# Kernel tuning notes

Hardware: AMD Instinct MI355X
Metric: run time of the kernel (lower is better)

## Reference

```python
import jax, jax.numpy as jnp
import numpy as np

B, T, C, NH = 8, 1024, 768, 12
HD = C // NH
NEG = -1e9


def setup_inputs() -> dict:
    key = jax.random.key(0)
    ks = jax.random.split(key, 8)
    s_c = 1.0 / np.sqrt(C)
    s_t = 1.0 / np.sqrt(T)
    return {
        "x": jax.random.normal(ks[0], (B, T, C), dtype=jnp.float32),
        "Wv": jax.random.normal(ks[1], (C, C), dtype=jnp.float32) * s_c,
        "bv": jnp.zeros((C,), dtype=jnp.float32),
        "Wl": jax.random.normal(ks[2], (T, T), dtype=jnp.float32) * s_t,  # weights_layer, no bias
        "Wc": jax.random.normal(ks[3], (T, T), dtype=jnp.float32) * s_t,  # weight_concat
        "bc": jnp.zeros((T,), dtype=jnp.float32),
        "Wp": jax.random.normal(ks[4], (C, C), dtype=jnp.float32) * s_c,
        "bp": jnp.zeros((C,), dtype=jnp.float32),
    }


def reference(x, Wv, bv, Wl, Wc, bc, Wp, bp):
    Bq, Tq, Cq = x.shape
    # NOTE: original forward uses self.value(x) for q, k, and v alike.
    v = x @ Wv.T + bv                              # [B,T,C]
    q = k = v
    # split heads -> [B, nh, T, hd]
    def heads(t):
        return t.reshape(Bq, Tq, NH, HD).transpose(0, 2, 1, 3)
    qh, kh, vh = heads(q), heads(k), heads(v)
    att = jnp.einsum("bhqd,bhkd->bhqk", qh, kh) / jnp.sqrt(jnp.float32(HD))
    # learned seqlen-mixing over the key dim: Linear(T,T) acts on last axis
    att = att @ Wl.T                               # weights_layer (no bias)
    att = att @ Wc.T + bc                          # weight_concat
    # causal mask (tril)
    causal = jnp.tril(jnp.ones((Tq, Tq), dtype=bool))
    att = jnp.where(causal[None, None], att, NEG)
    att = jax.nn.softmax(att, axis=-1)             # attn_drop is identity at eval
    y = jnp.einsum("bhqk,bhkd->bhqd", att, vh)
    y = y.transpose(0, 2, 1, 3).reshape(Bq, Tq, Cq)
    return y @ Wp.T + bp                           # resid_drop identity at eval
```

## Files before the change

kernel.cpp:

```cpp
#include <hip/hip_runtime.h>
#include <stdint.h>

#define Bz 8
#define Tz 1024
#define Cz 768
#define NHz 12
#define HDz 64

typedef unsigned short u16;
typedef __attribute__((ext_vector_type(8))) __bf16 bf16x8;
typedef __attribute__((ext_vector_type(4))) float f32x4;

__device__ __forceinline__ float bf2f(u16 b) {
    union { uint32_t u; float f; } c; c.u = ((uint32_t)b) << 16; return c.f;
}
__device__ __forceinline__ u16 f2bf(float f) {
    union { float f; uint32_t u; } c; c.f = f;
    uint32_t u = c.u;
    return (u16)((u + 0x7fffu + ((u >> 16) & 1u)) >> 16);
}

#define N4_X  (Bz * Tz * Cz / 4)
#define N4_WV (Cz * Cz / 4)
#define N4_WC (Tz * Tz / 4)
#define N4_WP (Cz * Cz / 4)
#define N4_ALL (N4_X + N4_WV + N4_WC + N4_WP)

__global__ __launch_bounds__(256)
void cvt_all(const float* __restrict__ x, const float* __restrict__ wv,
             const float* __restrict__ wc, const float* __restrict__ wp,
             u16* __restrict__ xb, u16* __restrict__ wvb,
             u16* __restrict__ wcb, u16* __restrict__ wpb) {
    int i = blockIdx.x * 256 + threadIdx.x;
    if (i >= N4_ALL) return;
    const float* in;
    u16* out;
    if (i < N4_X) {
        in = x; out = xb;
    } else if (i < N4_X + N4_WV) {
        in = wv; out = wvb; i -= N4_X;
    } else if (i < N4_X + N4_WV + N4_WC) {
        in = wc; out = wcb; i -= N4_X + N4_WV;
    } else {
        in = wp; out = wpb; i -= N4_X + N4_WV + N4_WC;
    }
    float4 v = ((const float4*)in)[i];
    union { u16 h[4]; uint2 u; } o;
    o.h[0] = f2bf(v.x); o.h[1] = f2bf(v.y); o.h[2] = f2bf(v.z); o.h[3] = f2bf(v.w);
    ((uint2*)out)[i] = o.u;
}

template<int BM, int BN, int WM, int WN, bool OUTF32, bool HASBIAS>
__global__ __launch_bounds__(WM * WN * 64)
void gemm_bt(const u16* __restrict__ A, long long sAz, int lda,
             const u16* __restrict__ Bp, long long sBz, int ldb,
             void* __restrict__ Cp, long long sCz, int ldc,
             const float* __restrict__ bias, int K, float alpha) {
    constexpr int NT = WM * WN * 64;
    constexpr int BK = 32;
    constexpr int AI = (BM * BK) / (NT * 8);
    constexpr int BI = (BN * BK) / (NT * 8);
    static_assert(AI >= 1 && (BM * BK) % (NT * 8) == 0, "A staging");
    static_assert(BI >= 1 && (BN * BK) % (NT * 8) == 0, "B staging");
    static_assert(BM == WM * 64 && BN == WN * 64, "wave tiling");

    __shared__ alignas(16) u16 As[2][BM * BK];
    __shared__ alignas(16) u16 Bs[2][BN * BK];

    const int z = blockIdx.z;
    const u16* Ag = A + (long long)z * sAz;
    const u16* Bg = Bp + (long long)z * sBz;

    const int tid = threadIdx.x;
    const int lane = tid & 63;
    const int w = tid >> 6;
    const int wm = w / WN;
    const int wn = w % WN;
    const int rowBase = blockIdx.y * BM;
    const int colBase = blockIdx.x * BN;
    const int koff = (lane >> 4) * 8;
    const int frow = lane & 15;

    auto stage = [&](int buf, int k0) {
#pragma unroll
        for (int i = 0; i < AI; i++) {
            int e = (i * NT + tid) * 8;
            const u16* g = Ag + (long long)(rowBase + (e >> 5)) * lda + k0 + (e & 31);
            __builtin_amdgcn_global_load_lds(
                (const __attribute__((address_space(1))) uint32_t*)g,
                (__attribute__((address_space(3))) uint32_t*)(&As[buf][0] + e), 16, 0, 0);
        }
#pragma unroll
        for (int i = 0; i < BI; i++) {
            int e = (i * NT + tid) * 8;
            const u16* g = Bg + (long long)(colBase + (e >> 5)) * ldb + k0 + (e & 31);
            __builtin_amdgcn_global_load_lds(
                (const __attribute__((address_space(1))) uint32_t*)g,
                (__attribute__((address_space(3))) uint32_t*)(&Bs[buf][0] + e), 16, 0, 0);
        }
    };

    f32x4 acc[4][4] = {};

    const int nk = K / BK;
    stage(0, 0);
    __syncthreads();

#pragma unroll 1
    for (int t = 0; t < nk; ++t) {
        const int cur = t & 1;
        if (t + 1 < nk) stage(cur ^ 1, (t + 1) * BK);

        bf16x8 af[4], bfr[4];
#pragma unroll
        for (int mt = 0; mt < 4; mt++)
            af[mt] = *(const bf16x8*)&As[cur][(wm * 64 + mt * 16 + frow) * BK + koff];
#pragma unroll
        for (int nt = 0; nt < 4; nt++)
            bfr[nt] = *(const bf16x8*)&Bs[cur][(wn * 64 + nt * 16 + frow) * BK + koff];
#pragma unroll
        for (int mt = 0; mt < 4; mt++)
#pragma unroll
            for (int nt = 0; nt < 4; nt++)
                acc[mt][nt] = __builtin_amdgcn_mfma_f32_16x16x32_bf16(
                    af[mt], bfr[nt], acc[mt][nt], 0, 0, 0);

        __syncthreads();
    }

    const int r0 = rowBase + wm * 64;
    const int c0 = colBase + wn * 64;
    const int rl = (lane >> 4) * 4;
    const int cl = lane & 15;
#pragma unroll
    for (int mt = 0; mt < 4; mt++) {
#pragma unroll
        for (int nt = 0; nt < 4; nt++) {
#pragma unroll
            for (int r = 0; r < 4; r++) {
                int row = r0 + mt * 16 + rl + r;
                int col = c0 + nt * 16 + cl;
                float v = acc[mt][nt][r] * alpha;
                if (HASBIAS) v += bias[col];
                if (OUTF32)
                    ((float*)Cp)[(long long)z * sCz + (long long)row * ldc + col] = v;
                else
                    ((u16*)Cp)[(long long)z * sCz + (long long)row * ldc + col] = f2bf(v);
            }
        }
    }
}

template<bool INF32>
__global__ __launch_bounds__(256)
void transpose_to_bf16(const void* __restrict__ in, u16* __restrict__ out,
                       int rows, int cols, long long sInZ, long long sOutZ) {
    __shared__ u16 tile[32][33];
    const int z = blockIdx.z;
    const int c0 = blockIdx.x * 32, r0 = blockIdx.y * 32;
    const int tx = threadIdx.x, ty = threadIdx.y;
#pragma unroll
    for (int i = 0; i < 32; i += 8) {
        long long off = (long long)z * sInZ + (long long)(r0 + ty + i) * cols + c0 + tx;
        tile[ty + i][tx] = INF32 ? f2bf(((const float*)in)[off]) : ((const u16*)in)[off];
    }
    __syncthreads();
#pragma unroll
    for (int i = 0; i < 32; i += 8)
        out[(long long)z * sOutZ + (long long)(c0 + ty + i) * rows + r0 + tx] = tile[tx][ty + i];
}

#define LOG2E 1.44269504f

__global__ __launch_bounds__(512)
void flash_attn(const u16* __restrict__ v, const u16* __restrict__ U,
                const u16* __restrict__ vT, const float* __restrict__ bc,
                u16* __restrict__ y) {
    __shared__ alignas(16) u16 Us[128 * 64];
    __shared__ alignas(16) u16 Vs[64 * 128];
    __shared__ alignas(16) u16 Ps[128 * 136];
    __shared__ u16 bcs[Tz];

    const int bi = blockIdx.x;
    const int xcd = bi & 7;
    const int slot = bi >> 3;
    const int col = (slot % 12) * 8 + xcd;
    const int qi = 7 - slot / 12;
    const int b = col / NHz, h = col % NHz;

    const int tid = threadIdx.x, lane = tid & 63, w = tid >> 6;
    const int quad = lane >> 4, cl = lane & 15;
    const int q0 = qi * 128;
    const int wrow = w * 16;

    for (int j = tid; j < Tz; j += 512) bcs[j] = f2bf(bc[j] * LOG2E);

    const u16* vq = v + ((long long)b * Tz + q0) * Cz + h * HDz;
    bf16x8 aS[2];
#pragma unroll
    for (int ks = 0; ks < 2; ks++)
        aS[ks] = *(const bf16x8*)(vq + (long long)(wrow + cl) * Cz + ks * 32 + quad * 8);

    f32x4 Oacc[4] = {};
    float mrow[4], lrow[4];
#pragma unroll
    for (int r = 0; r < 4; r++) { mrow[r] = -3.0e38f; lrow[r] = 0.f; }

    const u16* Ub = U + (long long)b * Tz * Cz + h * HDz;
    const u16* Vb = vT + ((long long)b * Cz + h * HDz) * Tz;

    __syncthreads();

    const int kts = qi + 1;
    for (int kt = 0; kt < kts; kt++) {
        if (kt) __builtin_amdgcn_s_barrier();
        const u16* Ug = Ub + (long long)kt * 128 * Cz;
#pragma unroll
        for (int i = 0; i < 2; i++) {
            int e = (i * 512 + tid) * 8;
            int key = e >> 6;
            int ch = ((e & 63) >> 3) ^ (key & 7);
            __builtin_amdgcn_global_load_lds(
                (const __attribute__((address_space(1))) uint32_t*)(Ug + (long long)key * Cz + ch * 8),
                (__attribute__((address_space(3))) uint32_t*)(Us + e), 16, 0, 0);
        }
        const u16* Vg = Vb + kt * 128;
#pragma unroll
        for (int i = 0; i < 2; i++) {
            int e = (i * 512 + tid) * 8;
            int dim = e >> 7;
            int ch = ((e & 127) >> 3) ^ (dim & 15);
            __builtin_amdgcn_global_load_lds(
                (const __attribute__((address_space(1))) uint32_t*)(Vg + (long long)dim * Tz + ch * 8),
                (__attribute__((address_space(3))) uint32_t*)(Vs + e), 16, 0, 0);
        }
        asm volatile("s_waitcnt vmcnt(2)" ::: "memory");
        __builtin_amdgcn_s_barrier();

        f32x4 S[8] = {};
        __builtin_amdgcn_s_setprio(1);
#pragma unroll
        for (int ks = 0; ks < 2; ks++)
#pragma unroll
            for (int nt = 0; nt < 8; nt++) {
                int key = nt * 16 + cl;
                bf16x8 bS = *(const bf16x8*)&Us[key * 64 + (((ks * 4 + quad) ^ (key & 7)) * 8)];
                S[nt] = __builtin_amdgcn_mfma_f32_16x16x32_bf16(aS[ks], bS, S[nt], 0, 0, 0);
            }
        __builtin_amdgcn_s_setprio(0);

        const bool last = (kt == kts - 1);
#pragma unroll
        for (int nt = 0; nt < 8; nt++) {
            float bl = bf2f(bcs[kt * 128 + nt * 16 + cl]);
#pragma unroll
            for (int r = 0; r < 4; r++) {
                int rowg = q0 + wrow + quad * 4 + r;
                int colg = kt * 128 + nt * 16 + cl;
                float s = S[nt][r] * (0.125f * LOG2E) + bl;
                if (last && colg > rowg) s = -3.0e38f;
                S[nt][r] = s;
            }
        }

        float mnew[4], alpha[4];
#pragma unroll
        for (int r = 0; r < 4; r++) {
            float m = S[0][r];
#pragma unroll
            for (int nt = 1; nt < 8; nt++) m = fmaxf(m, S[nt][r]);
#pragma unroll
            for (int d = 1; d < 16; d <<= 1) m = fmaxf(m, __shfl_xor(m, d));
            mnew[r] = fmaxf(mrow[r], m);
            alpha[r] = __builtin_amdgcn_exp2f(mrow[r] - mnew[r]);
            mrow[r] = mnew[r];
        }

        float psum[4] = {};
#pragma unroll
        for (int nt = 0; nt < 8; nt++)
#pragma unroll
            for (int r = 0; r < 4; r++) {
                float p = __builtin_amdgcn_exp2f(S[nt][r] - mnew[r]);
                psum[r] += p;
                Ps[(wrow + quad * 4 + r) * 136 + nt * 16 + cl] = f2bf(p);
            }
#pragma unroll
        for (int r = 0; r < 4; r++) {
            float s = psum[r];
#pragma unroll
            for (int d = 1; d < 16; d <<= 1) s += __shfl_xor(s, d);
            lrow[r] = lrow[r] * alpha[r] + s;
#pragma unroll
            for (int nt2 = 0; nt2 < 4; nt2++)
                Oacc[nt2][r] *= alpha[r];
        }

        asm volatile("s_waitcnt vmcnt(0)" ::: "memory");
        __builtin_amdgcn_s_barrier();

        __builtin_amdgcn_s_setprio(1);
#pragma unroll
        for (int ks = 0; ks < 4; ks++) {
            bf16x8 pA = *(const bf16x8*)&Ps[(wrow + cl) * 136 + ks * 32 + quad * 8];
#pragma unroll
            for (int nt2 = 0; nt2 < 4; nt2++) {
                int dim = nt2 * 16 + cl;
                bf16x8 vB = *(const bf16x8*)&Vs[dim * 128 + (((ks * 4 + quad) ^ cl) * 8)];
                Oacc[nt2] = __builtin_amdgcn_mfma_f32_16x16x32_bf16(pA, vB, Oacc[nt2], 0, 0, 0);
            }
        }
        __builtin_amdgcn_s_setprio(0);
    }

    u16* yq = y + ((long long)b * Tz + q0) * Cz + h * HDz;
#pragma unroll
    for (int r = 0; r < 4; r++) {
        float inv = 1.f / lrow[r];
#pragma unroll
        for (int nt2 = 0; nt2 < 4; nt2++)
            yq[(long long)(wrow + quad * 4 + r) * Cz + nt2 * 16 + cl] =
                f2bf(Oacc[nt2][r] * inv);
    }
}

extern "C" void kernel_launch(void* const* d_in, const int* in_sizes, int n_in,
                              void* d_out, int out_size, void* d_ws, size_t ws_size,
                              hipStream_t stream) {
    const float* x  = (const float*)d_in[0];
    const float* Wv = (const float*)d_in[1];
    const float* bv = (const float*)d_in[2];
    const float* Wl = (const float*)d_in[3];
    const float* Wc = (const float*)d_in[4];
    const float* bc = (const float*)d_in[5];
    const float* Wp = (const float*)d_in[6];
    const float* bp = (const float*)d_in[7];

    u16* ws  = (u16*)d_ws;
    u16* xb  = ws;
    u16* Wvb = xb  + (size_t)Bz * Tz * Cz;
    u16* Wcb = Wvb + (size_t)Cz * Cz;
    u16* Wpb = Wcb + (size_t)Tz * Tz;
    u16* WlT = Wpb + (size_t)Cz * Cz;
    u16* Wcl = WlT + (size_t)Tz * Tz;
    u16* vbf = Wcl + (size_t)Tz * Tz;
    u16* vT  = vbf + (size_t)Bz * Tz * Cz;
    u16* U   = vT  + (size_t)Bz * Tz * Cz;

    const long long sTC = (long long)Tz * Cz;
    const long long sCT = (long long)Cz * Tz;

    cvt_all<<<(N4_ALL + 255) / 256, 256, 0, stream>>>(x, Wv, Wc, Wp, xb, Wvb, Wcb, Wpb);
    transpose_to_bf16<true><<<dim3(32, 32, 1), dim3(32, 8), 0, stream>>>(Wl, WlT, Tz, Tz, 0, 0);
    gemm_bt<64, 64, 1, 1, false, false><<<dim3(Tz / 64, Tz / 64, 1), 64, 0, stream>>>(
        Wcb, 0, Tz, WlT, 0, Tz, Wcl, 0, Tz, nullptr, Tz, 1.f);
    gemm_bt<64, 128, 1, 2, false, true><<<dim3(Cz / 128, (Bz * Tz) / 64, 1), 128, 0, stream>>>(
        xb, 0, Cz, Wvb, 0, Cz, vbf, 0, Cz, bv, Cz, 1.f);
    transpose_to_bf16<false><<<dim3(Cz / 32, Tz / 32, Bz), dim3(32, 8), 0, stream>>>(
        vbf, vT, Tz, Cz, sTC, sCT);
    gemm_bt<64, 128, 1, 2, false, false><<<dim3(Cz / 128, Tz / 64, Bz), 128, 0, stream>>>(
        Wcl, 0, Tz, vT, sCT, Tz, U, sTC, Cz, nullptr, Tz, 1.f);
    flash_attn<<<dim3(8 * NHz * Bz, 1, 1), 512, 0, stream>>>(vbf, U, vT, bc, vbf);
    gemm_bt<64, 128, 1, 2, true, true><<<dim3(Cz / 128, (Bz * Tz) / 64, 1), 128, 0, stream>>>(
        vbf, 0, Cz, Wpb, 0, Cz, (float*)d_out, 0, Cz, bp, Cz, 1.f);
}
```

Before: 235.6 us.

## Widen GEMM K-tile with XOR-swizzled LDS, enlarge tiles, use hardware bf16 convert

The GEMM now stages 64-wide K slices into LDS with an XOR swizzle on the 8-element chunk index, which should cut bank conflicts and halve the number of barriers per K. The three large GEMMs move from 64x128 tiles with two waves to 128x128 tiles with four waves, raising data reuse per block. Float-to-bf16 rounding switches to the compiler's native conversion, and the causal mask in the attention kernel is pulled into a separate branch that runs only on the last key tile. The bigger tiles use more LDS and produce fewer blocks, which may lower occupancy, and the native conversion could round slightly differently.

Measured after the change: 221.3 us. -6.1%, faster.

```diff
diff --git a/kernel.cpp b/kernel.cpp
--- a/kernel.cpp
+++ b/kernel.cpp
@@ -10,6 +10,7 @@
 typedef unsigned short u16;
 typedef __attribute__((ext_vector_type(8))) __bf16 bf16x8;
 typedef __attribute__((ext_vector_type(4))) float f32x4;
+typedef __attribute__((ext_vector_type(4))) unsigned int u32x4;
 
 __device__ __forceinline__ float bf2f(u16 b) {
     union { uint32_t u; float f; } c; c.u = ((uint32_t)b) << 16; return c.f;
@@ -18,6 +19,10 @@
     union { float f; uint32_t u; } c; c.f = f;
     uint32_t u = c.u;
     return (u16)((u + 0x7fffu + ((u >> 16) & 1u)) >> 16);
+}
+__device__ __forceinline__ u16 f2bf_hw(float f) {
+    __bf16 b = (__bf16)f;
+    union { __bf16 b; u16 u; } c; c.b = b; return c.u;
 }
 
 #define N4_X  (Bz * Tz * Cz / 4)
@@ -57,7 +62,7 @@
              void* __restrict__ Cp, long long sCz, int ldc,
              const float* __restrict__ bias, int K, float alpha) {
     constexpr int NT = WM * WN * 64;
-    constexpr int BK = 32;
+    constexpr int BK = 64;
     constexpr int AI = (BM * BK) / (NT * 8);
     constexpr int BI = (BN * BK) / (NT * 8);
     static_assert(AI >= 1 && (BM * BK) % (NT * 8) == 0, "A staging");
@@ -78,14 +83,16 @@
     const int wn = w % WN;
     const int rowBase = blockIdx.y * BM;
     const int colBase = blockIdx.x * BN;
-    const int koff = (lane >> 4) * 8;
+    const int quad = lane >> 4;
     const int frow = lane & 15;
 
     auto stage = [&](int buf, int k0) {
 #pragma unroll
         for (int i = 0; i < AI; i++) {
             int e = (i * NT + tid) * 8;
-            const u16* g = Ag + (long long)(rowBase + (e >> 5)) * lda + k0 + (e & 31);
+            int row = e >> 6;
+            int gcol = (((e & 63) >> 3) ^ (row & 7)) * 8;
+            const u16* g = Ag + (long long)(rowBase + row) * lda + k0 + gcol;
             __builtin_amdgcn_global_load_lds(
                 (const __attribute__((address_space(1))) uint32_t*)g,
                 (__attribute__((address_space(3))) uint32_t*)(&As[buf][0] + e), 16, 0, 0);
@@ -93,7 +100,9 @@
 #pragma unroll
         for (int i = 0; i < BI; i++) {
             int e = (i * NT + tid) * 8;
-            const u16* g = Bg + (long long)(colBase + (e >> 5)) * ldb + k0 + (e & 31);
+            int row = e >> 6;
+            int gcol = (((e & 63) >> 3) ^ (row & 7)) * 8;
+            const u16* g = Bg + (long long)(colBase + row) * ldb + k0 + gcol;
             __builtin_amdgcn_global_load_lds(
                 (const __attribute__((address_space(1))) uint32_t*)g,
                 (__attribute__((address_space(3))) uint32_t*)(&Bs[buf][0] + e), 16, 0, 0);
@@ -111,19 +120,26 @@
         const int cur = t & 1;
         if (t + 1 < nk) stage(cur ^ 1, (t + 1) * BK);
 
-        bf16x8 af[4], bfr[4];
-#pragma unroll
-        for (int mt = 0; mt < 4; mt++)
-            af[mt] = *(const bf16x8*)&As[cur][(wm * 64 + mt * 16 + frow) * BK + koff];
-#pragma unroll
-        for (int nt = 0; nt < 4; nt++)
-            bfr[nt] = *(const bf16x8*)&Bs[cur][(wn * 64 + nt * 16 + frow) * BK + koff];
-#pragma unroll
-        for (int mt = 0; mt < 4; mt++)
-#pragma unroll
-            for (int nt = 0; nt < 4; nt++)
-                acc[mt][nt] = __builtin_amdgcn_mfma_f32_16x16x32_bf16(
-                    af[mt], bfr[nt], acc[mt][nt], 0, 0, 0);
+#pragma unroll
+        for (int kk = 0; kk < 2; kk++) {
+            bf16x8 af[4], bfr[4];
+#pragma unroll
+            for (int mt = 0; mt < 4; mt++) {
+                int row = wm * 64 + mt * 16 + frow;
+                af[mt] = *(const bf16x8*)&As[cur][row * 64 + (((kk * 4 + quad) ^ (frow & 7)) * 8)];
+            }
+#pragma unroll
+            for (int nt = 0; nt < 4; nt++) {
+                int row = wn * 64 + nt * 16 + frow;
+                bfr[nt] = *(const bf16x8*)&Bs[cur][row * 64 + (((kk * 4 + quad) ^ (frow & 7)) * 8)];
+            }
+#pragma unroll
+            for (int mt = 0; mt < 4; mt++)
+#pragma unroll
+                for (int nt = 0; nt < 4; nt++)
+                    acc[mt][nt] = __builtin_amdgcn_mfma_f32_16x16x32_bf16(
+                        af[mt], bfr[nt], acc[mt][nt], 0, 0, 0);
+        }
 
         __syncthreads();
     }
@@ -145,7 +161,7 @@
                 if (OUTF32)
                     ((float*)Cp)[(long long)z * sCz + (long long)row * ldc + col] = v;
                 else
-                    ((u16*)Cp)[(long long)z * sCz + (long long)row * ldc + col] = f2bf(v);
+                    ((u16*)Cp)[(long long)z * sCz + (long long)row * ldc + col] = f2bf_hw(v);
             }
         }
     }
@@ -254,12 +270,17 @@
         for (int nt = 0; nt < 8; nt++) {
             float bl = bf2f(bcs[kt * 128 + nt * 16 + cl]);
 #pragma unroll
-            for (int r = 0; r < 4; r++) {
-                int rowg = q0 + wrow + quad * 4 + r;
+            for (int r = 0; r < 4; r++)
+                S[nt][r] = S[nt][r] * (0.125f * LOG2E) + bl;
+        }
+        if (last) {
+            int rowg = q0 + wrow + quad * 4;
+#pragma unroll
+            for (int nt = 0; nt < 8; nt++) {
                 int colg = kt * 128 + nt * 16 + cl;
-                float s = S[nt][r] * (0.125f * LOG2E) + bl;
-                if (last && colg > rowg) s = -3.0e38f;
-                S[nt][r] = s;
+#pragma unroll
+                for (int r = 0; r < 4; r++)
+                    if (colg > rowg + r) S[nt][r] = -3.0e38f;
             }
         }
 
@@ -283,7 +304,7 @@
             for (int r = 0; r < 4; r++) {
                 float p = __builtin_amdgcn_exp2f(S[nt][r] - mnew[r]);
                 psum[r] += p;
-                Ps[(wrow + quad * 4 + r) * 136 + nt * 16 + cl] = f2bf(p);
+                Ps[(wrow + quad * 4 + r) * 136 + nt * 16 + cl] = f2bf_hw(p);
             }
 #pragma unroll
         for (int r = 0; r < 4; r++) {
@@ -320,7 +341,7 @@
 #pragma unroll
         for (int nt2 = 0; nt2 < 4; nt2++)
             yq[(long long)(wrow + quad * 4 + r) * Cz + nt2 * 16 + cl] =
-                f2bf(Oacc[nt2][r] * inv);
+                f2bf_hw(Oacc[nt2][r] * inv);
     }
 }
 
@@ -354,13 +375,13 @@
     transpose_to_bf16<true><<<dim3(32, 32, 1), dim3(32, 8), 0, stream>>>(Wl, WlT, Tz, Tz, 0, 0);
     gemm_bt<64, 64, 1, 1, false, false><<<dim3(Tz / 64, Tz / 64, 1), 64, 0, stream>>>(
         Wcb, 0, Tz, WlT, 0, Tz, Wcl, 0, Tz, nullptr, Tz, 1.f);
-    gemm_bt<64, 128, 1, 2, false, true><<<dim3(Cz / 128, (Bz * Tz) / 64, 1), 128, 0, stream>>>(
+    gemm_bt<128, 128, 2, 2, false, true><<<dim3(Cz / 128, (Bz * Tz) / 128, 1), 256, 0, stream>>>(
         xb, 0, Cz, Wvb, 0, Cz, vbf, 0, Cz, bv, Cz, 1.f);
     transpose_to_bf16<false><<<dim3(Cz / 32, Tz / 32, Bz), dim3(32, 8), 0, stream>>>(
         vbf, vT, Tz, Cz, sTC, sCT);
-    gemm_bt<64, 128, 1, 2, false, false><<<dim3(Cz / 128, Tz / 64, Bz), 128, 0, stream>>>(
+    gemm_bt<128, 128, 2, 2, false, false><<<dim3(Cz / 128, Tz / 128, Bz), 256, 0, stream>>>(
         Wcl, 0, Tz, vT, sCT, Tz, U, sTC, Cz, nullptr, Tz, 1.f);
     flash_attn<<<dim3(8 * NHz * Bz, 1, 1), 512, 0, stream>>>(vbf, U, vT, bc, vbf);
-    gemm_bt<64, 128, 1, 2, true, true><<<dim3(Cz / 128, (Bz * Tz) / 64, 1), 128, 0, stream>>>(
+    gemm_bt<128, 128, 2, 2, true, true><<<dim3(Cz / 128, (Bz * Tz) / 128, 1), 256, 0, stream>>>(
         vbf, 0, Cz, Wpb, 0, Cz, (float*)d_out, 0, Cz, bp, Cz, 1.f);
 }
```
